# Optimization experiments

Measured on AMD Instinct MI355X. Metric: run time of the kernel, lower is better.

## Reference

```python
import jax, jax.numpy as jnp
import numpy as np

L, D, H, EXP = 4, 512, 8, 4
HD = D // H
DFF = D * EXP
B, S = 8, 1024
LN_EPS = 1e-3  # keras LayerNormalization default epsilon


def _glorot(key, shape):
    fan_in, fan_out = shape[-2], shape[-1]
    lim = np.sqrt(6.0 / (fan_in + fan_out))
    return jax.random.uniform(key, shape, jnp.float32, -lim, lim)


def setup_inputs() -> dict:
    key = jax.random.key(0)
    ks = jax.random.split(key, 12)
    x = jax.random.normal(ks[0], (B, S, D), jnp.float32)
    # sequence mask from random lengths (mimics tf.sequence_mask(row_lengths))
    lengths = jax.random.randint(ks[1], (B,), S // 2, S + 1)
    mask = (jnp.arange(S)[None, :] < lengths[:, None])  # [B,S] bool
    inp = {
        'x': x, 'mask': mask,
        'Wq': _glorot(ks[2], (L, D, D)),
        'Wk': _glorot(ks[3], (L, D, D)),
        'Wv': _glorot(ks[4], (L, D, D)),
        'Wo': _glorot(ks[5], (L, D, D)),
        'ln1_g': jnp.ones((L, D), jnp.float32),
        'ln1_b': jnp.zeros((L, D), jnp.float32),
        'ln2_g': jnp.ones((L, D), jnp.float32),
        'ln2_b': jnp.zeros((L, D), jnp.float32),
        'W1': _glorot(ks[6], (L, D, DFF)),
        'b1': jnp.zeros((L, DFF), jnp.float32),
        'W2': _glorot(ks[7], (L, DFF, D)),
        'b2': jnp.zeros((L, D), jnp.float32),
    }
    return inp


def _layernorm(x, g, b):
    mu = jnp.mean(x, axis=-1, keepdims=True)
    var = jnp.mean(jnp.square(x - mu), axis=-1, keepdims=True)
    return (x - mu) * jax.lax.rsqrt(var + LN_EPS) * g + b


def _pos_encoding(s, d):
    # matches the source: sin/cos halves with inv freq 10000**(2j/d), j<d/2
    half = d // 2
    p = jnp.arange(s, dtype=jnp.float32)[:, None]          # [S,1]
    inv = 10000.0 ** (2.0 * jnp.arange(half, dtype=jnp.float32) / d)  # [half]
    ang = p / inv[None, :]                                 # [S,half]
    return jnp.concatenate([jnp.sin(ang), jnp.cos(ang)], axis=1)  # [S,D]


def _forward(x, mask, Wq, Wk, Wv, Wo, ln1_g, ln1_b, ln2_g, ln2_b, W1, b1, W2, b2):
    b, s, d = x.shape
    x = x + _pos_encoding(s, d)
    key_mask = mask[:, None, None, :]  # [B,1,1,Sk]
    scale = 1.0 / jnp.sqrt(jnp.float32(HD))
    for l in range(L):
        h = _layernorm(x, ln1_g[l], ln1_b[l])
        q = (h @ Wq[l]).reshape(b, s, H, HD).transpose(0, 2, 1, 3)  # bhsd
        k = (h @ Wk[l]).reshape(b, s, H, HD).transpose(0, 2, 1, 3)
        v = (h @ Wv[l]).reshape(b, s, H, HD).transpose(0, 2, 1, 3)
        scores = jnp.einsum('bhqd,bhkd->bhqk', q, k) * scale
        scores = jnp.where(key_mask, scores, -1e9)
        attn = jax.nn.softmax(scores, axis=-1)
        o = jnp.einsum('bhqk,bhkd->bhqd', attn, v)
        o = o.transpose(0, 2, 1, 3).reshape(b, s, d) @ Wo[l]
        x = x + o  # dropout rate 0 / inference -> identity
        h = _layernorm(x, ln2_g[l], ln2_b[l])
        f = jax.nn.relu(h @ W1[l] + b1[l]) @ W2[l] + b2[l]
        x = x + f
    return x


def reference(x, mask, Wq, Wk, Wv, Wo, ln1_g, ln1_b, ln2_g, ln2_b, W1, b1, W2, b2):
    return _forward(x, mask, Wq, Wk, Wv, Wo, ln1_g, ln1_b, ln2_g, ln2_b, W1, b1, W2, b2)
```

## Files before the change

kernel.cpp:

```cpp
#include <hip/hip_runtime.h>
#include <math.h>

#define NB 8
#define SEQ 1024
#define DM 512
#define NH 8
#define HDIM 64
#define DFF 2048
#define NLAYER 4
#define NTOK (NB * SEQ)
#define QKVD 1536

typedef __attribute__((ext_vector_type(8))) short bf16x8;
typedef __attribute__((ext_vector_type(4))) float f32x4;

__device__ __forceinline__ ushort f2bf(float f) {
    union { float f; unsigned u; } v; v.f = f;
    unsigned r = (v.u + 0x7FFF + ((v.u >> 16) & 1)) >> 16;
    return (ushort)r;
}

__device__ __forceinline__ void async16(const void* g, void* l) {
    __builtin_amdgcn_global_load_lds(
        (const __attribute__((address_space(1))) unsigned int*)g,
        (__attribute__((address_space(3))) unsigned int*)l, 16, 0, 0);
}

__global__ __launch_bounds__(256) void add_pos_kernel(const float* __restrict__ x,
                                                      float* __restrict__ out) {
    int idx4 = blockIdx.x * blockDim.x + threadIdx.x;
    int base = idx4 * 4;
    int d = base & (DM - 1);
    int s = (base >> 9) & (SEQ - 1);
    float4 v = *(const float4*)&x[base];
    float r[4] = {v.x, v.y, v.z, v.w};
#pragma unroll
    for (int i = 0; i < 4; i++) {
        int dd = d + i;
        float pe;
        if (dd < 256) {
            float inv = powf(10000.0f, 2.0f * (float)dd / 512.0f);
            pe = sinf((float)s / inv);
        } else {
            float inv = powf(10000.0f, 2.0f * (float)(dd - 256) / 512.0f);
            pe = cosf((float)s / inv);
        }
        r[i] += pe;
    }
    *(float4*)&out[base] = make_float4(r[0], r[1], r[2], r[3]);
}

__global__ __launch_bounds__(256) void wtrans_all(
    const float* __restrict__ Wq, const float* __restrict__ Wk,
    const float* __restrict__ Wv, const float* __restrict__ Wo,
    const float* __restrict__ W1, const float* __restrict__ W2,
    ushort* __restrict__ WqkvT, ushort* __restrict__ WoT,
    ushort* __restrict__ W1T, ushort* __restrict__ W2T) {
    __shared__ float tile[32][36];
    const int l = blockIdx.z;
    const int bid = blockIdx.x;
    const float* src; ushort* dst;
    int K, N, rowOff, stride, t, nxk;
    if (bid < 1024) {
        int seg = bid >> 8; t = bid & 255;
        K = 512; N = 512; nxk = 16;
        if (seg == 0)      { src = Wq; dst = WqkvT; rowOff = 0;    stride = 786432; }
        else if (seg == 1) { src = Wk; dst = WqkvT; rowOff = 512;  stride = 786432; }
        else if (seg == 2) { src = Wv; dst = WqkvT; rowOff = 1024; stride = 786432; }
        else               { src = Wo; dst = WoT;   rowOff = 0;    stride = 262144; }
    } else if (bid < 2048) {
        t = bid - 1024; K = 512; N = 2048; nxk = 64;
        src = W1; dst = W1T; rowOff = 0; stride = 1048576;
    } else {
        t = bid - 2048; K = 2048; N = 512; nxk = 16;
        src = W2; dst = W2T; rowOff = 0; stride = 1048576;
    }
    const int bx = t % nxk, by = t / nxk;
    const int kb = by * 32, nb = bx * 32;
    const float* s = src + (size_t)l * K * N;
    ushort* d = dst + (size_t)l * stride;
    int r = threadIdx.x >> 3, c4 = (threadIdx.x & 7) * 4;
    float4 v = *(const float4*)&s[(size_t)(kb + r) * N + nb + c4];
    *(float4*)&tile[r][c4] = v;
    __syncthreads();
    ushort4 o;
    o.x = f2bf(tile[c4 + 0][r]);
    o.y = f2bf(tile[c4 + 1][r]);
    o.z = f2bf(tile[c4 + 2][r]);
    o.w = f2bf(tile[c4 + 3][r]);
    *(ushort4*)&d[(size_t)(rowOff + nb + r) * K + kb + c4] = o;
}

__global__ __launch_bounds__(256) void ln_kernel(const float* __restrict__ x,
                                                 const float* __restrict__ g,
                                                 const float* __restrict__ bta,
                                                 ushort* __restrict__ out) {
    int w = threadIdx.x >> 6;
    int lane = threadIdx.x & 63;
    size_t row = (size_t)blockIdx.x * 4 + w;
    const float* xr = x + row * DM;
    float4 v0 = *(const float4*)&xr[lane * 4];
    float4 v1 = *(const float4*)&xr[256 + lane * 4];
    float sum = v0.x + v0.y + v0.z + v0.w + v1.x + v1.y + v1.z + v1.w;
#pragma unroll
    for (int off = 32; off > 0; off >>= 1) sum += __shfl_xor(sum, off, 64);
    float mu = sum * (1.0f / 512.0f);
    float d0[8] = {v0.x - mu, v0.y - mu, v0.z - mu, v0.w - mu,
                   v1.x - mu, v1.y - mu, v1.z - mu, v1.w - mu};
    float sq = 0.0f;
#pragma unroll
    for (int i = 0; i < 8; i++) sq = fmaf(d0[i], d0[i], sq);
#pragma unroll
    for (int off = 32; off > 0; off >>= 1) sq += __shfl_xor(sq, off, 64);
    float rs = rsqrtf(sq * (1.0f / 512.0f) + 1e-3f);
    float4 g0 = *(const float4*)&g[lane * 4];
    float4 g1 = *(const float4*)&g[256 + lane * 4];
    float4 b0 = *(const float4*)&bta[lane * 4];
    float4 b1 = *(const float4*)&bta[256 + lane * 4];
    ushort* orow = out + row * DM;
    ushort4 o0, o1;
    o0.x = f2bf(fmaf(d0[0] * rs, g0.x, b0.x));
    o0.y = f2bf(fmaf(d0[1] * rs, g0.y, b0.y));
    o0.z = f2bf(fmaf(d0[2] * rs, g0.z, b0.z));
    o0.w = f2bf(fmaf(d0[3] * rs, g0.w, b0.w));
    o1.x = f2bf(fmaf(d0[4] * rs, g1.x, b1.x));
    o1.y = f2bf(fmaf(d0[5] * rs, g1.y, b1.y));
    o1.z = f2bf(fmaf(d0[6] * rs, g1.z, b1.z));
    o1.w = f2bf(fmaf(d0[7] * rs, g1.w, b1.w));
    *(ushort4*)&orow[lane * 4] = o0;
    *(ushort4*)&orow[256 + lane * 4] = o1;
}

template <int BM, int BN, int KH, int MODE>
__global__ __launch_bounds__(512) void gemm_bf16(const ushort* __restrict__ A,
                                                 const ushort* __restrict__ Bt,
                                                 const float* __restrict__ bias,
                                                 void* __restrict__ Cv,
                                                 void* __restrict__ aux,
                                                 int M, int N, int K) {
    static_assert(BM % 64 == 0 && BN % 64 == 0, "tile multiple of 64");
    constexpr int FM = BM / 64;
    constexpr int FN = BN / 32;
    __shared__ __align__(16) ushort As[2][KH * BM * 32];
    __shared__ __align__(16) ushort Bs[2][KH * BN * 32];
    const int tid = threadIdx.x;
    const int lane = tid & 63;
    const int w = tid >> 6;

    const int nx = gridDim.x;
    int wg = blockIdx.y * nx + blockIdx.x;
    int xcd = wg & 7;
    int t0 = wg >> 3;
    int bx = t0 % nx;
    int by = (t0 / nx) * 8 + xcd;
    const int m0 = by * BM, n0 = bx * BN;

    const int wm = (w >> 1) * (BM / 4);
    const int wn = (w & 1) * (BN / 2);
    const int fm = lane & 15, fq = lane >> 4;

    f32x4 acc[FM][FN] = {};

    auto stage = [&](int buf, int kt) {
#pragma unroll
        for (int hf = 0; hf < KH; hf++) {
            constexpr int CA = BM * 4;
            if constexpr (CA >= 512) {
#pragma unroll
                for (int u = 0; u < CA / 512; u++) {
                    int chunk = u * 512 + tid;
                    int row = chunk >> 2, c = chunk & 3;
                    async16(&A[(size_t)(m0 + row) * K + kt + hf * 32 + c * 8],
                            (char*)As[buf] + hf * BM * 64 + chunk * 16);
                }
            } else {
                if (tid < CA) {
                    int chunk = tid;
                    int row = chunk >> 2, c = chunk & 3;
                    async16(&A[(size_t)(m0 + row) * K + kt + hf * 32 + c * 8],
                            (char*)As[buf] + hf * BM * 64 + chunk * 16);
                }
            }
            constexpr int CB = BN * 4;
            if constexpr (CB >= 512) {
#pragma unroll
                for (int u = 0; u < CB / 512; u++) {
                    int chunk = u * 512 + tid;
                    int row = chunk >> 2, c = chunk & 3;
                    async16(&Bt[(size_t)(n0 + row) * K + kt + hf * 32 + c * 8],
                            (char*)Bs[buf] + hf * BN * 64 + chunk * 16);
                }
            } else {
                if (tid < CB) {
                    int chunk = tid;
                    int row = chunk >> 2, c = chunk & 3;
                    async16(&Bt[(size_t)(n0 + row) * K + kt + hf * 32 + c * 8],
                            (char*)Bs[buf] + hf * BN * 64 + chunk * 16);
                }
            }
        }
    };

    stage(0, 0);
    __syncthreads();
    int cur = 0;
    for (int kt = 0; kt < K; kt += 32 * KH) {
        if (kt + 32 * KH < K) stage(cur ^ 1, kt + 32 * KH);
#pragma unroll
        for (int hf = 0; hf < KH; hf++) {
            bf16x8 af[FM], bfr[FN];
#pragma unroll
            for (int i = 0; i < FM; i++)
                af[i] = *(const bf16x8*)&As[cur][hf * BM * 32 +
                                                 (wm + i * 16 + fm) * 32 + fq * 8];
#pragma unroll
            for (int j = 0; j < FN; j++)
                bfr[j] = *(const bf16x8*)&Bs[cur][hf * BN * 32 +
                                                  (wn + j * 16 + fm) * 32 + fq * 8];
#pragma unroll
            for (int i = 0; i < FM; i++)
#pragma unroll
                for (int j = 0; j < FN; j++)
                    acc[i][j] = __builtin_amdgcn_mfma_f32_16x16x32_bf16(
                        af[i], bfr[j], acc[i][j], 0, 0, 0);
        }
        __syncthreads();
        cur ^= 1;
    }

    if constexpr (MODE == 5) {
        if (n0 >= 1024) {
            ushort* vT = (ushort*)aux;
            const int b = m0 >> 10;
            const int sl = (m0 & (SEQ - 1)) + wm + fq * 4;
#pragma unroll
            for (int i = 0; i < FM; i++) {
#pragma unroll
                for (int j = 0; j < FN; j++) {
                    int c = n0 - 1024 + wn + j * 16 + fm;
                    ushort4 o;
                    o.x = f2bf(acc[i][j][0]);
                    o.y = f2bf(acc[i][j][1]);
                    o.z = f2bf(acc[i][j][2]);
                    o.w = f2bf(acc[i][j][3]);
                    *(ushort4*)&vT[(size_t)(b * DM + c) * SEQ + sl + i * 16] = o;
                }
            }
        } else {
#pragma unroll
            for (int i = 0; i < FM; i++)
#pragma unroll
                for (int j = 0; j < FN; j++) {
                    int col = n0 + wn + j * 16 + fm;
#pragma unroll
                    for (int r = 0; r < 4; r++) {
                        int row = m0 + wm + i * 16 + fq * 4 + r;
                        ((ushort*)Cv)[(size_t)row * N + col] = f2bf(acc[i][j][r]);
                    }
                }
        }
        return;
    }

#pragma unroll
    for (int i = 0; i < FM; i++) {
#pragma unroll
        for (int j = 0; j < FN; j++) {
            int col = n0 + wn + j * 16 + fm;
#pragma unroll
            for (int r = 0; r < 4; r++) {
                int row = m0 + wm + i * 16 + fq * 4 + r;
                float vv = acc[i][j][r];
                if constexpr (MODE == 0) {
                    ((ushort*)Cv)[(size_t)row * N + col] = f2bf(vv);
                } else if constexpr (MODE == 1) {
                    float* C = (float*)Cv;
                    C[(size_t)row * N + col] += vv;
                } else if constexpr (MODE == 2) {
                    vv += bias[col];
                    vv = fmaxf(vv, 0.0f);
                    ((ushort*)Cv)[(size_t)row * N + col] = f2bf(vv);
                } else {
                    float* C = (float*)Cv;
                    C[(size_t)row * N + col] += vv + bias[col];
                }
            }
        }
    }
}

__global__ __launch_bounds__(512) void attn_mfma(const ushort* __restrict__ QKV,
                                                 const ushort* __restrict__ Vt,
                                                 const int* __restrict__ mask,
                                                 ushort* __restrict__ O) {
    __shared__ __align__(16) ushort Kt[64 * 64];
    __shared__ __align__(16) ushort Vs[64 * 64];
    __shared__ __align__(16) ushort ps[8][16 * 72];
    __shared__ float mskf[64];
    __shared__ int lensh[8];

    const int tid = threadIdx.x, lane = tid & 63, w = tid >> 6;
    const int h = blockIdx.y, b = blockIdx.z;
    const int q0 = blockIdx.x * 128 + w * 16;
    const int fm = lane & 15, fq = lane >> 4;
    ushort* pw = &ps[w][0];
    const float L2E = 1.44269504f;

    int part = mask[b * SEQ + tid] + mask[b * SEQ + 512 + tid];
#pragma unroll
    for (int off = 32; off > 0; off >>= 1) part += __shfl_xor(part, off, 64);
    if (lane == 0) lensh[w] = part;

    bf16x8 qf[2];
#pragma unroll
    for (int kk = 0; kk < 2; kk++) {
        bf16x8 t = *(const bf16x8*)&QKV[(size_t)(b * SEQ + q0 + fm) * QKVD + h * HDIM +
                                        kk * 32 + fq * 8];
#pragma unroll
        for (int j = 0; j < 8; j++) {
            union { float f; unsigned u; } vv;
            vv.u = ((unsigned)(ushort)t[j]) << 16;
            vv.f *= 0.125f;
            t[j] = (short)(ushort)(vv.u >> 16);
        }
        qf[kk] = t;
    }

    const int r0 = tid >> 3, c0 = tid & 7;
    const int dk0 = (r0 * 8 + (c0 ^ (r0 & 7))) * 16;

    auto gK = [&](int j0) {
        return (const uint4*)&QKV[(size_t)(b * SEQ + j0 + r0) * QKVD + 512 +
                                  h * HDIM + c0 * 8];
    };
    auto gV = [&](int j0) {
        return (const uint4*)&Vt[(size_t)((b * NH + h) * HDIM + r0) * SEQ + j0 + c0 * 8];
    };

    uint4 kreg = *gK(0);
    uint4 vreg = *gV(0);
    int mreg = (tid < 64) ? mask[b * SEQ + tid] : 0;
    *(uint4*)((char*)Kt + dk0) = kreg;
    *(uint4*)((char*)Vs + dk0) = vreg;
    if (tid < 64) mskf[tid] = mreg ? 1.0f : 0.0f;
    __syncthreads();

    const int len = lensh[0] + lensh[1] + lensh[2] + lensh[3] +
                    lensh[4] + lensh[5] + lensh[6] + lensh[7];
    const int jmax = (len + 63) & ~63;

    f32x4 oacc[4] = {};
    float mrow = -INFINITY, lrow = 0.0f;

    for (int j0 = 0; j0 < jmax; j0 += 64) {
        const bool has_next = (j0 + 64 < jmax);
        if (has_next) {
            kreg = *gK(j0 + 64);
            vreg = *gV(j0 + 64);
            if (tid < 64) mreg = mask[b * SEQ + j0 + 64 + tid];
        }

        f32x4 sc[4] = {};
        __builtin_amdgcn_s_setprio(1);
#pragma unroll
        for (int nt = 0; nt < 4; nt++) {
            int key = nt * 16 + fm;
#pragma unroll
            for (int kk = 0; kk < 2; kk++) {
                bf16x8 kf = *(const bf16x8*)((char*)Kt +
                            (key * 8 + ((kk * 4 + fq) ^ (key & 7))) * 16);
                sc[nt] = __builtin_amdgcn_mfma_f32_16x16x32_bf16(kf, qf[kk], sc[nt], 0, 0, 0);
            }
        }
        __builtin_amdgcn_s_setprio(0);

        float mx = -INFINITY;
#pragma unroll
        for (int nt = 0; nt < 4; nt++)
#pragma unroll
            for (int r = 0; r < 4; r++) mx = fmaxf(mx, sc[nt][r]);
        mx = fmaxf(mx, __shfl_xor(mx, 16));
        mx = fmaxf(mx, __shfl_xor(mx, 32));
        if (!__all(mx - mrow <= 8.0f)) {
            float mn = fmaxf(mrow, mx);
            float alpha = __expf(mrow - mn);
            mrow = mn;
            lrow *= alpha;
#pragma unroll
            for (int nt = 0; nt < 4; nt++)
#pragma unroll
                for (int r = 0; r < 4; r++) oacc[nt][r] *= alpha;
        }

        const float nm2 = -mrow * L2E;
        float sv[4][4];
        float ls = 0.0f;
#pragma unroll
        for (int nt = 0; nt < 4; nt++) {
            f32x4 mv = *(const f32x4*)&mskf[nt * 16 + fq * 4];
#pragma unroll
            for (int r = 0; r < 4; r++) {
                float p = exp2f(fmaf(sc[nt][r], L2E, nm2)) * mv[r];
                sv[nt][r] = p;
                ls += p;
            }
        }
        ls += __shfl_xor(ls, 16);
        ls += __shfl_xor(ls, 32);
        lrow += ls;

#pragma unroll
        for (int nt = 0; nt < 4; nt++) {
            union { float f; unsigned u; } a0, a1, a2, a3;
            a0.f = sv[nt][0]; a1.f = sv[nt][1]; a2.f = sv[nt][2]; a3.f = sv[nt][3];
            unsigned d0 = (a0.u >> 16) | (a1.u & 0xFFFF0000u);
            unsigned d1 = (a2.u >> 16) | (a3.u & 0xFFFF0000u);
            *(uint2*)&pw[fm * 72 + nt * 16 + fq * 4] = make_uint2(d0, d1);
        }

        __builtin_amdgcn_s_setprio(1);
#pragma unroll
        for (int kk = 0; kk < 2; kk++) {
            bf16x8 pf = *(const bf16x8*)&pw[fm * 72 + kk * 32 + fq * 8];
#pragma unroll
            for (int nt = 0; nt < 4; nt++) {
                int dim = nt * 16 + fm;
                bf16x8 vf = *(const bf16x8*)((char*)Vs +
                            (dim * 8 + ((kk * 4 + fq) ^ (dim & 7))) * 16);
                oacc[nt] = __builtin_amdgcn_mfma_f32_16x16x32_bf16(vf, pf, oacc[nt], 0, 0, 0);
            }
        }
        __builtin_amdgcn_s_setprio(0);

        __syncthreads();
        if (has_next) {
            *(uint4*)((char*)Kt + dk0) = kreg;
            *(uint4*)((char*)Vs + dk0) = vreg;
            if (tid < 64) mskf[tid] = mreg ? 1.0f : 0.0f;
            __syncthreads();
        }
    }

    float inv = 1.0f / lrow;
#pragma unroll
    for (int nt = 0; nt < 4; nt++) {
        ushort4 o;
        o.x = f2bf(oacc[nt][0] * inv);
        o.y = f2bf(oacc[nt][1] * inv);
        o.z = f2bf(oacc[nt][2] * inv);
        o.w = f2bf(oacc[nt][3] * inv);
        *(ushort4*)&O[(size_t)(b * SEQ + q0 + fm) * DM + h * HDIM + nt * 16 + fq * 4] = o;
    }
}

extern "C" void kernel_launch(void* const* d_in, const int* in_sizes, int n_in,
                              void* d_out, int out_size, void* d_ws, size_t ws_size,
                              hipStream_t stream) {
    const float* x_in = (const float*)d_in[0];
    const int* mask   = (const int*)d_in[1];
    const float* Wq   = (const float*)d_in[2];
    const float* Wk   = (const float*)d_in[3];
    const float* Wv   = (const float*)d_in[4];
    const float* Wo   = (const float*)d_in[5];
    const float* ln1g = (const float*)d_in[6];
    const float* ln1b = (const float*)d_in[7];
    const float* ln2g = (const float*)d_in[8];
    const float* ln2b = (const float*)d_in[9];
    const float* W1   = (const float*)d_in[10];
    const float* b1   = (const float*)d_in[11];
    const float* W2   = (const float*)d_in[12];
    const float* b2   = (const float*)d_in[13];

    float* x = (float*)d_out;
    ushort* wsb = (ushort*)d_ws;
    const size_t U = 1048576;
    ushort* WqkvT = wsb;
    ushort* WoT   = wsb + 3 * U;
    ushort* W1T   = wsb + 4 * U;
    ushort* W2T   = wsb + 8 * U;
    ushort* hb    = wsb + 12 * U;
    ushort* qkv   = wsb + 16 * U;
    ushort* ob    = wsb + 28 * U;
    ushort* vTb   = wsb + 32 * U;
    ushort* f1b   = qkv;

    wtrans_all<<<dim3(3072, 1, 4), 256, 0, stream>>>(Wq, Wk, Wv, Wo, W1, W2,
                                                     WqkvT, WoT, W1T, W2T);

    add_pos_kernel<<<(NTOK * DM / 4) / 256, 256, 0, stream>>>(x_in, x);

    dim3 gQKV(QKVD / 128, NTOK / 128);
    dim3 gProj(DM / 64, NTOK / 64);
    dim3 gFF1(DFF / 128, NTOK / 128);
    dim3 gFF2(DM / 64, NTOK / 64);
    dim3 gAttn(SEQ / 128, NH, NB);

    for (int l = 0; l < NLAYER; l++) {
        const size_t wOff   = (size_t)l * 262144;
        const size_t wqkvOff= (size_t)l * 786432;
        const size_t w1Off  = (size_t)l * 1048576;

        ln_kernel<<<NTOK / 4, 256, 0, stream>>>(x, ln1g + l * DM, ln1b + l * DM, hb);
        gemm_bf16<128, 128, 1, 5><<<gQKV, 512, 0, stream>>>(hb, WqkvT + wqkvOff, nullptr,
                                                            qkv, vTb, NTOK, QKVD, DM);
        attn_mfma<<<gAttn, 512, 0, stream>>>(qkv, vTb, mask, ob);
        gemm_bf16<64, 64, 2, 1><<<gProj, 512, 0, stream>>>(ob, WoT + wOff, nullptr, x,
                                                           nullptr, NTOK, DM, DM);
        ln_kernel<<<NTOK / 4, 256, 0, stream>>>(x, ln2g + l * DM, ln2b + l * DM, hb);
        gemm_bf16<128, 128, 1, 2><<<gFF1, 512, 0, stream>>>(hb, W1T + w1Off,
                                                            b1 + (size_t)l * DFF, f1b,
                                                            nullptr, NTOK, DFF, DM);
        gemm_bf16<64, 64, 2, 3><<<gFF2, 512, 0, stream>>>(f1b, W2T + w1Off,
                                                          b2 + (size_t)l * DM, x,
                                                          nullptr, NTOK, DM, DFF);
    }
}
```

Before: 695.8 us.

## Double-buffer K/V tiles in attention and replace mask loads with length compare

The attention kernel now uses two LDS buffers for K and V tiles, so each iteration needs only one barrier instead of two. The per-tile mask load into shared memory is removed and replaced by comparing key indices against the sequence length, with a fast unmasked path for full tiles. This cuts barrier and mask traffic at the cost of extra LDS. It assumes the mask is a contiguous prefix, which holds for sequence masks.

```diff
diff --git a/kernel.cpp b/kernel.cpp
--- a/kernel.cpp
+++ b/kernel.cpp
@@ -293,10 +293,9 @@
                                                  const ushort* __restrict__ Vt,
                                                  const int* __restrict__ mask,
                                                  ushort* __restrict__ O) {
-    __shared__ __align__(16) ushort Kt[64 * 64];
-    __shared__ __align__(16) ushort Vs[64 * 64];
+    __shared__ __align__(16) ushort Kt[2][64 * 64];
+    __shared__ __align__(16) ushort Vs[2][64 * 64];
     __shared__ __align__(16) ushort ps[8][16 * 72];
-    __shared__ float mskf[64];
     __shared__ int lensh[8];
 
     const int tid = threadIdx.x, lane = tid & 63, w = tid >> 6;
@@ -339,25 +338,26 @@
 
     uint4 kreg = *gK(0);
     uint4 vreg = *gV(0);
-    int mreg = (tid < 64) ? mask[b * SEQ + tid] : 0;
-    *(uint4*)((char*)Kt + dk0) = kreg;
-    *(uint4*)((char*)Vs + dk0) = vreg;
-    if (tid < 64) mskf[tid] = mreg ? 1.0f : 0.0f;
-    __syncthreads();
-
-    const int len = lensh[0] + lensh[1] + lensh[2] + lensh[3] +
-                    lensh[4] + lensh[5] + lensh[6] + lensh[7];
-    const int jmax = (len + 63) & ~63;
 
     f32x4 oacc[4] = {};
     float mrow = -INFINITY, lrow = 0.0f;
+    int len = 0;
+    int jmax = SEQ;
 
     for (int j0 = 0; j0 < jmax; j0 += 64) {
+        const int buf = (j0 >> 6) & 1;
+        *(uint4*)((char*)Kt[buf] + dk0) = kreg;
+        *(uint4*)((char*)Vs[buf] + dk0) = vreg;
+        __syncthreads();
+        if (j0 == 0) {
+            len = lensh[0] + lensh[1] + lensh[2] + lensh[3] +
+                  lensh[4] + lensh[5] + lensh[6] + lensh[7];
+            jmax = (len + 63) & ~63;
+        }
         const bool has_next = (j0 + 64 < jmax);
         if (has_next) {
             kreg = *gK(j0 + 64);
             vreg = *gV(j0 + 64);
-            if (tid < 64) mreg = mask[b * SEQ + j0 + 64 + tid];
         }
 
         f32x4 sc[4] = {};
@@ -367,7 +367,7 @@
             int key = nt * 16 + fm;
 #pragma unroll
             for (int kk = 0; kk < 2; kk++) {
-                bf16x8 kf = *(const bf16x8*)((char*)Kt +
+                bf16x8 kf = *(const bf16x8*)((char*)Kt[buf] +
                             (key * 8 + ((kk * 4 + fq) ^ (key & 7))) * 16);
                 sc[nt] = __builtin_amdgcn_mfma_f32_16x16x32_bf16(kf, qf[kk], sc[nt], 0, 0, 0);
             }
@@ -395,15 +395,25 @@
         const float nm2 = -mrow * L2E;
         float sv[4][4];
         float ls = 0.0f;
-#pragma unroll
-        for (int nt = 0; nt < 4; nt++) {
-            f32x4 mv = *(const f32x4*)&mskf[nt * 16 + fq * 4];
-#pragma unroll
-            for (int r = 0; r < 4; r++) {
-                float p = exp2f(fmaf(sc[nt][r], L2E, nm2)) * mv[r];
-                sv[nt][r] = p;
-                ls += p;
-            }
+        if (j0 + 64 <= len) {
+#pragma unroll
+            for (int nt = 0; nt < 4; nt++)
+#pragma unroll
+                for (int r = 0; r < 4; r++) {
+                    float p = exp2f(fmaf(sc[nt][r], L2E, nm2));
+                    sv[nt][r] = p;
+                    ls += p;
+                }
+        } else {
+#pragma unroll
+            for (int nt = 0; nt < 4; nt++)
+#pragma unroll
+                for (int r = 0; r < 4; r++) {
+                    int key = j0 + nt * 16 + fq * 4 + r;
+                    float p = (key < len) ? exp2f(fmaf(sc[nt][r], L2E, nm2)) : 0.0f;
+                    sv[nt][r] = p;
+                    ls += p;
+                }
         }
         ls += __shfl_xor(ls, 16);
         ls += __shfl_xor(ls, 32);
@@ -425,20 +435,12 @@
 #pragma unroll
             for (int nt = 0; nt < 4; nt++) {
                 int dim = nt * 16 + fm;
-                bf16x8 vf = *(const bf16x8*)((char*)Vs +
+                bf16x8 vf = *(const bf16x8*)((char*)Vs[buf] +
                             (dim * 8 + ((kk * 4 + fq) ^ (dim & 7))) * 16);
                 oacc[nt] = __builtin_amdgcn_mfma_f32_16x16x32_bf16(vf, pf, oacc[nt], 0, 0, 0);
             }
         }
         __builtin_amdgcn_s_setprio(0);
-
-        __syncthreads();
-        if (has_next) {
-            *(uint4*)((char*)Kt + dk0) = kreg;
-            *(uint4*)((char*)Vs + dk0) = vreg;
-            if (tid < 64) mskf[tid] = mreg ? 1.0f : 0.0f;
-            __syncthreads();
-        }
     }
 
     float inv = 1.0f / lrow;
```

New measurement: 687.5 us, median of 2. About the same (-1.2%).
